# Performance work log

Measured on AMD Instinct MI355X. Metric: run time of the kernel, lower is better.

## Reference

```python
import jax, jax.numpy as jnp
import numpy as np

VOCAB = 1_000_000      # max_vocabulary_size_per_gpu (use_hashtable=False -> direct index)
EMB = 64               # embedding_vec_size
BATCH = 4096
SLOTS = 26             # slot_num
MAX_NNZ = 10           # max_nnz per slot
COMBINER = "mean"     # 'mean' or 'sum'


def setup_inputs() -> dict:
    key = jax.random.key(0)
    k1, k2, k3 = jax.random.split(key, 3)
    keys = jax.random.randint(k1, (BATCH, SLOTS, MAX_NNZ), 0, VOCAB, dtype=jnp.int32)
    # validity mask: models SparseTensor ragged structure (padded to max_nnz)
    mask = jax.random.uniform(k2, (BATCH, SLOTS, MAX_NNZ)) < 0.6
    # default initializer: random_uniform(-0.05, 0.05)
    table = jax.random.uniform(k3, (VOCAB, EMB), minval=-0.05, maxval=0.05, dtype=jnp.float32)
    return {"keys": keys, "mask": mask, "table": table}


def reference(keys, mask, table):
    # gather: [B, S, N, E]; zero out padded slots
    gathered = table[keys] * mask[..., None].astype(table.dtype)
    summed = jnp.sum(gathered, axis=2)  # [B, S, E]
    if COMBINER == "mean":
        counts = jnp.maximum(jnp.sum(mask, axis=2), 1).astype(table.dtype)  # [B, S]
        return summed / counts[..., None]
    return summed
```

## Files before the change

### kernel.cpp

```cpp
#include <hip/hip_runtime.h>

#define BATCH   4096
#define SLOTS   26
#define MAX_NNZ 10
#define EMB     64
#define ROWS    (BATCH * SLOTS)

typedef float floatx4 __attribute__((ext_vector_type(4)));

__global__ __launch_bounds__(256) void emb_fwd_kernel(
    const int*   __restrict__ keys,
    const int*   __restrict__ mask,
    const float* __restrict__ table,
    float*       __restrict__ out)
{
    int tid = blockIdx.x * blockDim.x + threadIdx.x;
    int row = tid >> 4;
    int e4  = tid & 15;
    if (row >= ROWS) return;

    const int* kp = keys + (size_t)row * MAX_NNZ;
    const int* mp = mask + (size_t)row * MAX_NNZ;

    int kk[MAX_NNZ];
    int mm[MAX_NNZ];
#pragma unroll
    for (int j = 0; j < MAX_NNZ; ++j) kk[j] = kp[j];
#pragma unroll
    for (int j = 0; j < MAX_NNZ; ++j) mm[j] = mp[j];

#pragma unroll
    for (int j = 0; j < MAX_NNZ; ++j) {
        kk[j] = mm[j] ? kk[j] : 0;
    }

    floatx4 v[MAX_NNZ];
#pragma unroll
    for (int j = 0; j < MAX_NNZ; ++j) {
        const floatx4* rowp = (const floatx4*)(table + (size_t)kk[j] * EMB);
        v[j] = rowp[e4];
    }

    floatx4 acc = (floatx4){0.f, 0.f, 0.f, 0.f};
    int cnt = 0;
#pragma unroll
    for (int j = 0; j < MAX_NNZ; ++j) {
        float w = (float)(mm[j] != 0);
        cnt += (mm[j] != 0);
        acc += w * v[j];
    }

    float inv = 1.0f / (float)(cnt > 0 ? cnt : 1);
    acc *= inv;

    floatx4* op = (floatx4*)(out + (size_t)row * EMB) + e4;
    __builtin_nontemporal_store(acc, op);
}

extern "C" void kernel_launch(void* const* d_in, const int* in_sizes, int n_in,
                              void* d_out, int out_size, void* d_ws, size_t ws_size,
                              hipStream_t stream) {
    const int*   keys  = (const int*)d_in[0];
    const int*   mask  = (const int*)d_in[1];
    const float* table = (const float*)d_in[2];
    float*       out   = (float*)d_out;

    const int threads_per_row = 16;
    const int block = 256;
    const long long total_threads = (long long)ROWS * threads_per_row;
    const int grid = (int)((total_threads + block - 1) / block);

    emb_fwd_kernel<<<grid, block, 0, stream>>>(keys, mask, table, out);
}
```

Baseline: 329.3 us.

## Use 32 threads per row with float2 loads and 32-bit byte offsets

Each row is now handled by 32 threads, each loading float2 instead of float4. Gather addresses are built as 32-bit byte offsets (key<<8), which fits because the table is 256 MB. Masked entries still point at row 0, and instead of a per-entry multiply by the mask weight, a single correction subtracts (MAX_NNZ-cnt) times row 0 from the summed result. A launch-bounds occupancy hint and a tree reduction are also added. The intent is more memory-level parallelism and fewer address instructions, at the cost of twice as many threads and small float differences from the subtraction correction.

```diff
diff --git a/kernel.cpp b/kernel.cpp
--- a/kernel.cpp
+++ b/kernel.cpp
@@ -6,54 +6,54 @@
 #define EMB     64
 #define ROWS    (BATCH * SLOTS)
 
-typedef float floatx4 __attribute__((ext_vector_type(4)));
+typedef float floatx2 __attribute__((ext_vector_type(2)));
 
-__global__ __launch_bounds__(256) void emb_fwd_kernel(
+__global__ __launch_bounds__(256, 8) void emb_fwd_kernel(
     const int*   __restrict__ keys,
     const int*   __restrict__ mask,
     const float* __restrict__ table,
     float*       __restrict__ out)
 {
     int tid = blockIdx.x * blockDim.x + threadIdx.x;
-    int row = tid >> 4;
-    int e4  = tid & 15;
+    int row = tid >> 5;
+    int e2  = tid & 31;
     if (row >= ROWS) return;
 
-    const int* kp = keys + (size_t)row * MAX_NNZ;
-    const int* mp = mask + (size_t)row * MAX_NNZ;
+    const int* kp = keys + row * MAX_NNZ;
+    const int* mp = mask + row * MAX_NNZ;
 
-    int kk[MAX_NNZ];
-    int mm[MAX_NNZ];
-#pragma unroll
-    for (int j = 0; j < MAX_NNZ; ++j) kk[j] = kp[j];
-#pragma unroll
-    for (int j = 0; j < MAX_NNZ; ++j) mm[j] = mp[j];
-
-#pragma unroll
-    for (int j = 0; j < MAX_NNZ; ++j) {
-        kk[j] = mm[j] ? kk[j] : 0;
-    }
-
-    floatx4 v[MAX_NNZ];
-#pragma unroll
-    for (int j = 0; j < MAX_NNZ; ++j) {
-        const floatx4* rowp = (const floatx4*)(table + (size_t)kk[j] * EMB);
-        v[j] = rowp[e4];
-    }
-
-    floatx4 acc = (floatx4){0.f, 0.f, 0.f, 0.f};
+    unsigned off[MAX_NNZ];
     int cnt = 0;
 #pragma unroll
     for (int j = 0; j < MAX_NNZ; ++j) {
-        float w = (float)(mm[j] != 0);
-        cnt += (mm[j] != 0);
-        acc += w * v[j];
+        int k = kp[j];
+        int m = mp[j];
+        cnt += (m != 0);
+        off[j] = ((unsigned)(m ? k : 0)) << 8;
     }
 
-    float inv = 1.0f / (float)(cnt > 0 ? cnt : 1);
-    acc *= inv;
+    const char* tb = (const char*)table;
+    unsigned e8 = (unsigned)e2 * 8u;
 
-    floatx4* op = (floatx4*)(out + (size_t)row * EMB) + e4;
+    floatx2 r0 = *(const floatx2*)(tb + e8);
+    floatx2 v[MAX_NNZ];
+#pragma unroll
+    for (int j = 0; j < MAX_NNZ; ++j) {
+        v[j] = *(const floatx2*)(tb + (off[j] + e8));
+    }
+
+    floatx2 s01 = v[0] + v[1];
+    floatx2 s23 = v[2] + v[3];
+    floatx2 s45 = v[4] + v[5];
+    floatx2 s67 = v[6] + v[7];
+    floatx2 s89 = v[8] + v[9];
+    floatx2 acc = ((s01 + s23) + (s45 + s67)) + s89;
+
+    float miss = (float)(MAX_NNZ - cnt);
+    float inv  = 1.0f / (float)(cnt > 0 ? cnt : 1);
+    acc = (acc - miss * r0) * inv;
+
+    floatx2* op = (floatx2*)(out + (size_t)row * EMB) + e2;
     __builtin_nontemporal_store(acc, op);
 }
 
@@ -65,7 +65,7 @@
     const float* table = (const float*)d_in[2];
     float*       out   = (float*)d_out;
 
-    const int threads_per_row = 16;
+    const int threads_per_row = 32;
     const int block = 256;
     const long long total_threads = (long long)ROWS * threads_per_row;
     const int grid = (int)((total_threads + block - 1) / block);
```

Result: slower. 338.1 us (+2.7%).
